# Kernel optimization log

Hardware: AMD Instinct MI355X
Metric: run time of the kernel (lower is better)

The kernel has to match this reference:

```python
import jax, jax.numpy as jnp
import numpy as np

H = 64
N_PERSON = 200000
N_MOVIE = 100000
E_ACTED = 1600000
E_DIRECTED = 200000
E_WWW = 3200000
N_LAYERS = 2


def setup_inputs() -> dict:
    key = jax.random.key(0)
    ks = jax.random.split(key, 24)
    s = 1.0 / np.sqrt(H)
    inp = {
        "x_person": jax.random.normal(ks[0], (N_PERSON, H), jnp.float32),
        "x_movie": jax.random.normal(ks[1], (N_MOVIE, H), jnp.float32),
        "acted_src": jax.random.randint(ks[2], (E_ACTED,), 0, N_PERSON, jnp.int32),
        "acted_dst": jax.random.randint(ks[3], (E_ACTED,), 0, N_MOVIE, jnp.int32),
        "directed_src": jax.random.randint(ks[4], (E_DIRECTED,), 0, N_PERSON, jnp.int32),
        "directed_dst": jax.random.randint(ks[5], (E_DIRECTED,), 0, N_MOVIE, jnp.int32),
        "www_src": jax.random.randint(ks[6], (E_WWW,), 0, N_PERSON, jnp.int32),
        "www_dst": jax.random.randint(ks[7], (E_WWW,), 0, N_PERSON, jnp.int32),
        # per-relation SAGEConv params, stacked over the 2 layers
        "Wl_acted": jax.random.normal(ks[8], (N_LAYERS, H, H), jnp.float32) * s,
        "bl_acted": jnp.zeros((N_LAYERS, H), jnp.float32),
        "Wr_acted": jax.random.normal(ks[9], (N_LAYERS, H, H), jnp.float32) * s,
        "Wl_directed": jax.random.normal(ks[10], (N_LAYERS, H, H), jnp.float32) * s,
        "bl_directed": jnp.zeros((N_LAYERS, H), jnp.float32),
        "Wr_directed": jax.random.normal(ks[11], (N_LAYERS, H, H), jnp.float32) * s,
        "Wl_www": jax.random.normal(ks[12], (N_LAYERS, H, H), jnp.float32) * s,
        "bl_www": jnp.zeros((N_LAYERS, H), jnp.float32),
        "Wr_www": jax.random.normal(ks[13], (N_LAYERS, H, H), jnp.float32) * s,
        "lin_W": jax.random.normal(ks[14], (1, H), jnp.float32) * s,
        "lin_b": jnp.zeros((1,), jnp.float32),
    }
    return inp


def sage_conv(x_src, x_dst, src, dst, Wl, bl, Wr, n_dst):
    # PyG SAGEConv: mean-aggregate source feats at dst, then lin_l(agg) + lin_r(x_dst)
    agg = jax.ops.segment_sum(x_src[src], dst, num_segments=n_dst)  # [n_dst, H_in]
    cnt = jax.ops.segment_sum(jnp.ones((src.shape[0],), x_src.dtype), dst, num_segments=n_dst)
    mean = agg / jnp.maximum(cnt, 1.0)[:, None]
    return mean @ Wl.T + bl + x_dst @ Wr.T


def reference(x_person, x_movie, acted_src, acted_dst, directed_src, directed_dst,
              www_src, www_dst, Wl_acted, bl_acted, Wr_acted,
              Wl_directed, bl_directed, Wr_directed,
              Wl_www, bl_www, Wr_www, lin_W, lin_b):
    x_p, x_m = x_person, x_movie
    for l in range(N_LAYERS):
        # HeteroConv(aggr='sum'): movie receives sum of acted_in and directed convs
        out_m = sage_conv(x_p, x_m, acted_src, acted_dst,
                          Wl_acted[l], bl_acted[l], Wr_acted[l], N_MOVIE)
        out_m = out_m + sage_conv(x_p, x_m, directed_src, directed_dst,
                                  Wl_directed[l], bl_directed[l], Wr_directed[l], N_MOVIE)
        out_p = sage_conv(x_p, x_p, www_src, www_dst,
                          Wl_www[l], bl_www[l], Wr_www[l], N_PERSON)
        x_m = jax.nn.relu(out_m)
        x_p = jax.nn.relu(out_p)
    return (x_m @ lin_W.T + lin_b).squeeze(-1)  # [N_MOVIE]
```

## Files before the change

### kernel.cpp

```cpp
#include <hip/hip_runtime.h>

#define H 64
#define N_PERSON 200000
#define N_MOVIE 100000
#define E_ACTED 1600000
#define E_DIRECTED 200000
#define E_WWW 3200000
#define E_TOTAL (E_ACTED + E_DIRECTED + E_WWW)

#define SH 11
#define NBIN 2048
#define CH 16384

typedef __attribute__((ext_vector_type(8))) short bf16x8;
typedef __attribute__((ext_vector_type(4))) float f32x4;

static __device__ __forceinline__ ushort f2bf(float f) {
  uint u = __float_as_uint(f);
  uint r = (u + 0x7FFFu + ((u >> 16) & 1u)) >> 16;
  return (ushort)r;
}
static __device__ __forceinline__ float bflo(uint u) { return __uint_as_float(u << 16); }
static __device__ __forceinline__ float bfhiq(uint u) { return __uint_as_float(u); }
static __device__ __forceinline__ uint packbf(float lo, float hi) {
  return (uint)f2bf(lo) | ((uint)f2bf(hi) << 16);
}


struct RelP {
  const int* src; const int* dst; int* off;
  int E, N, nblk, nbuk, blkbase, bukbase, cbase, ebase;
};


static __global__ __launch_bounds__(256) void count_cast_k(RelP a, RelP b, RelP c,
                                                           int* __restrict__ counts, int castbase,
                                                           const float* __restrict__ i0,
                                                           ushort* __restrict__ o0, int n0,
                                                           const float* __restrict__ i1,
                                                           ushort* __restrict__ o1, int n1) {
  int blk = blockIdx.x, t = threadIdx.x;
  if (blk >= castbase) {
    int i = (blk - castbase) * 256 + t;
    int stride = 2048 * 256;
    int nt = n0 + n1;
    for (; i < nt; i += stride) {
      const float4* in; ushort4* out; int idx;
      if (i < n0) { in = (const float4*)i0; out = (ushort4*)o0; idx = i; }
      else { in = (const float4*)i1; out = (ushort4*)o1; idx = i - n0; }
      float4 v = in[idx];
      ushort4 o;
      o.x = f2bf(v.x); o.y = f2bf(v.y); o.z = f2bf(v.z); o.w = f2bf(v.w);
      out[idx] = o;
    }
    return;
  }
  __shared__ int hist[128];
  RelP r = (blk >= c.blkbase) ? c : (blk >= b.blkbase) ? b : a;
  int lb = blk - r.blkbase;
  for (int i = t; i < r.nbuk; i += 256) hist[i] = 0;
  __syncthreads();
  int e0 = lb * CH, e1 = min(e0 + CH, r.E);
  for (int e = e0 + t; e < e1; e += 256) atomicAdd(&hist[r.dst[e] >> SH], 1);
  __syncthreads();
  for (int i = t; i < r.nbuk; i += 256) counts[r.cbase + i * r.nblk + lb] = hist[i];
}


static __global__ __launch_bounds__(1024) void scan_one_k(const int* __restrict__ in, int n,
                                                          int* __restrict__ out, int total) {
  __shared__ int wsum[16];
  int t = threadIdx.x;
  int C = (n + 1023) / 1024;
  int i0 = t * C, i1 = min(i0 + C, n);
  int s = 0;
  for (int i = i0; i < i1; ++i) s += in[i];
  int lane = t & 63, w = t >> 6;
  int incl = s;
  for (int d = 1; d < 64; d <<= 1) {
    int v = __shfl_up(incl, d, 64);
    if (lane >= d) incl += v;
  }
  if (lane == 63) wsum[w] = incl;
  __syncthreads();
  if (t == 0) {
    int acc = 0;
    for (int i = 0; i < 16; ++i) { int v = wsum[i]; wsum[i] = acc; acc += v; }
  }
  __syncthreads();
  int run = wsum[w] + (incl - s);
  for (int i = i0; i < i1; ++i) { int v = in[i]; out[i] = run; run += v; }
  if (t == 0) out[n] = total;
}


static __global__ __launch_bounds__(256) void part_scatter_all_k(RelP a, RelP b, RelP c,
                                                                 const int* __restrict__ off_bb,
                                                                 int* __restrict__ pairs) {
  __shared__ int cur[128];
  int blk = blockIdx.x, t = threadIdx.x;
  RelP r = (blk >= c.blkbase) ? c : (blk >= b.blkbase) ? b : a;
  int lb = blk - r.blkbase;
  for (int i = t; i < r.nbuk; i += 256) cur[i] = off_bb[r.cbase + i * r.nblk + lb];
  __syncthreads();
  int e0 = lb * CH, e1 = min(e0 + CH, r.E);
  int e = e0 + t;
  for (; e + 256 < e1; e += 512) {
    int d0 = r.dst[e], s0 = r.src[e];
    int d1 = r.dst[e + 256], s1 = r.src[e + 256];
    int p0 = atomicAdd(&cur[d0 >> SH], 1);
    int p1 = atomicAdd(&cur[d1 >> SH], 1);
    pairs[p0] = ((d0 & (NBIN - 1)) << 18) | s0;
    pairs[p1] = ((d1 & (NBIN - 1)) << 18) | s1;
  }
  if (e < e1) {
    int d0 = r.dst[e], s0 = r.src[e];
    int p0 = atomicAdd(&cur[d0 >> SH], 1);
    pairs[p0] = ((d0 & (NBIN - 1)) << 18) | s0;
  }
}


static __global__ __launch_bounds__(1024) void fine_sort_all_k(RelP a, RelP b, RelP c,
                                                               const int* __restrict__ off_bb,
                                                               const int* __restrict__ pairs,
                                                               int* __restrict__ csr) {
  __shared__ int hist[NBIN];
  __shared__ int wsum[16];
  int bb = blockIdx.x, t = threadIdx.x;
  RelP r = (bb >= c.bukbase) ? c : (bb >= b.bukbase) ? b : a;
  int bkt = bb - r.bukbase;
  int bstart = off_bb[r.cbase + bkt * r.nblk];
  int bend = (bkt + 1 < r.nbuk) ? off_bb[r.cbase + (bkt + 1) * r.nblk] : (r.ebase + r.E);
  int base = bkt << SH;
  int b0 = t * 2, b1 = t * 2 + 1;
  hist[b0] = 0; hist[b1] = 0;
  __syncthreads();
  for (int e = bstart + t; e < bend; e += 1024) atomicAdd(&hist[((uint)pairs[e]) >> 18], 1);
  __syncthreads();
  int h0 = hist[b0], h1 = hist[b1];
  int s = h0 + h1;
  int lane = t & 63, w = t >> 6;
  int incl = s;
  for (int d = 1; d < 64; d <<= 1) {
    int v = __shfl_up(incl, d, 64);
    if (lane >= d) incl += v;
  }
  if (lane == 63) wsum[w] = incl;
  __syncthreads();
  if (t == 0) {
    int acc = 0;
    for (int i = 0; i < 16; ++i) { int v = wsum[i]; wsum[i] = acc; acc += v; }
  }
  __syncthreads();
  int excl = wsum[w] + (incl - s);
  int ex0 = excl, ex1 = excl + h0;
  if (base + b0 < r.N) r.off[base + b0] = bstart + ex0;
  if (base + b1 < r.N) r.off[base + b1] = bstart + ex1;
  if (bkt == r.nbuk - 1 && t == 0) r.off[r.N] = r.ebase + r.E;
  hist[b0] = ex0; hist[b1] = ex1;
  __syncthreads();
  for (int e = bstart + t; e < bend; e += 1024) {
    int p = pairs[e];
    int pos = bstart + atomicAdd(&hist[((uint)p) >> 18], 1);
    csr[pos] = p & 0x3FFFF;
  }
}


struct PullT { const ushort* xsrc; const int* off; ushort* mean; int n; int blkbase; };

#define ACC8(u)                                  \
  do {                                           \
    a0 += bflo((u).x); a1 += bfhiq((u).x);       \
    a2 += bflo((u).y); a3 += bfhiq((u).y);       \
    a4 += bflo((u).z); a5 += bfhiq((u).z);       \
    a6 += bflo((u).w); a7 += bfhiq((u).w);       \
  } while (0)

static __global__ __launch_bounds__(256) void pull_all_k(PullT t0, PullT t1, PullT t2,
                                                         const int* __restrict__ csr) {
  int blk = blockIdx.x;
  PullT tk;
  if (t2.n > 0 && blk >= t2.blkbase) tk = t2;
  else if (blk >= t1.blkbase) tk = t1;
  else tk = t0;
  int lane = threadIdx.x & 63;
  int g = lane >> 3;
  int fo = lane & 7;
  int d = ((blk - tk.blkbase) * 4 + (threadIdx.x >> 6)) * 8 + g;
  bool dok = d < tk.n;
  int dd = dok ? d : (tk.n - 1);
  int e0 = tk.off[dd];
  int e1 = tk.off[dd + 1];
  int cnt = dok ? (e1 - e0) : 0;
  int mx = cnt;
  mx = max(mx, __shfl_xor(mx, 8, 64));
  mx = max(mx, __shfl_xor(mx, 16, 64));
  mx = max(mx, __shfl_xor(mx, 32, 64));

  const ushort* __restrict__ xrow = tk.xsrc + fo * 8;
  float a0 = 0.f, a1 = 0.f, a2 = 0.f, a3 = 0.f, a4 = 0.f, a5 = 0.f, a6 = 0.f, a7 = 0.f;

  int i = 0;
  for (; i + 2 <= mx; i += 2) {
    if (i + 1 < cnt) {
      int s0 = csr[e0 + i];
      int s1 = csr[e0 + i + 1];
      uint4 u0 = *(const uint4*)(xrow + (size_t)s0 * 64);
      uint4 u1 = *(const uint4*)(xrow + (size_t)s1 * 64);
      ACC8(u0); ACC8(u1);
    } else if (i < cnt) {
      int s0 = csr[e0 + i];
      uint4 u0 = *(const uint4*)(xrow + (size_t)s0 * 64);
      ACC8(u0);
    }
  }
  if (i < mx && i < cnt) {
    int s0 = csr[e0 + i];
    uint4 u0 = *(const uint4*)(xrow + (size_t)s0 * 64);
    ACC8(u0);
  }

  if (dok) {
    float inv = 1.0f / fmaxf((float)cnt, 1.0f);
    uint4 o;
    o.x = packbf(a0 * inv, a1 * inv);
    o.y = packbf(a2 * inv, a3 * inv);
    o.z = packbf(a4 * inv, a5 * inv);
    o.w = packbf(a6 * inv, a7 * inv);
    *(uint4*)(tk.mean + (size_t)d * 64 + fo * 8) = o;
  }
}


struct GemmT {
  const ushort *A0, *A1, *A2;
  const float *W0, *W1, *W2, *Wadd, *b0, *b1;
  ushort* outB;
  const float *projW, *projb;
  float* projOut;
  int M, nsrc, blkbase;
};

static __global__ __launch_bounds__(256) void gemm_all_k(GemmT g0, GemmT g1) {
  GemmT g = (g1.M > 0 && (int)blockIdx.x >= g1.blkbase) ? g1 : g0;
  __shared__ ushort Wt[3][64][72];
  const int t = threadIdx.x;
  const int w = t >> 6;
  const int l = t & 63;
  const int lr = l & 15;
  const int lk = l >> 4;
  const int m0 = ((int)blockIdx.x - g.blkbase) * 256;

  auto stageW = [&](const float* W, int s, const float* Wa) {
#pragma unroll
    for (int i = 0; i < 8; ++i) {
      int dp = t + i * 256;
      int j = dp >> 5;
      int kk = (dp & 31) * 2;
      float2 wv = *(const float2*)(W + j * 64 + kk);
      if (Wa) {
        float2 av = *(const float2*)(Wa + j * 64 + kk);
        wv.x += av.x; wv.y += av.y;
      }
      *(uint*)&Wt[s][j][kk] = packbf(wv.x, wv.y);
    }
  };
  stageW(g.W0, 0, nullptr);
  stageW(g.W1, 1, g.nsrc == 2 ? g.Wadd : nullptr);
  if (g.nsrc > 2) stageW(g.W2, 2, g.Wadd);
  __syncthreads();

  f32x4 acc[4][4];
#pragma unroll
  for (int mt = 0; mt < 4; ++mt)
#pragma unroll
    for (int jt = 0; jt < 4; ++jt) acc[mt][jt] = (f32x4){0.f, 0.f, 0.f, 0.f};

  auto doSrc = [&](const ushort* A, int s) {
    bf16x8 aF[4][2];
#pragma unroll
    for (int mt = 0; mt < 4; ++mt) {
      int m = m0 + w * 64 + mt * 16 + lr;
      const ushort* ap = A + (size_t)(m < g.M ? m : 0) * 64 + lk * 8;
      aF[mt][0] = *(const bf16x8*)(ap);
      aF[mt][1] = *(const bf16x8*)(ap + 32);
    }
#pragma unroll
    for (int jt = 0; jt < 4; ++jt) {
#pragma unroll
      for (int k0 = 0; k0 < 2; ++k0) {
        bf16x8 bF = *(const bf16x8*)&Wt[s][jt * 16 + lr][k0 * 32 + lk * 8];
#pragma unroll
        for (int mt = 0; mt < 4; ++mt)
          acc[mt][jt] =
              __builtin_amdgcn_mfma_f32_16x16x32_bf16(bF, aF[mt][k0], acc[mt][jt], 0, 0, 0);
      }
    }
  };
  doSrc(g.A0, 0);
  doSrc(g.A1, 1);
  if (g.nsrc > 2) doSrc(g.A2, 2);

  f32x4 bv[4];
#pragma unroll
  for (int jt = 0; jt < 4; ++jt) {
    f32x4 b = (f32x4){0.f, 0.f, 0.f, 0.f};
    if (g.b0) b += *(const f32x4*)(g.b0 + jt * 16 + lk * 4);
    if (g.b1) b += *(const f32x4*)(g.b1 + jt * 16 + lk * 4);
    bv[jt] = b;
  }

  if (g.projOut) {
    f32x4 pw[4];
#pragma unroll
    for (int jt = 0; jt < 4; ++jt) pw[jt] = *(const f32x4*)(g.projW + jt * 16 + lk * 4);
    float pb = g.projb[0];
#pragma unroll
    for (int mt = 0; mt < 4; ++mt) {
      float p = 0.f;
#pragma unroll
      for (int jt = 0; jt < 4; ++jt) {
        f32x4 o = acc[mt][jt] + bv[jt];
#pragma unroll
        for (int q = 0; q < 4; ++q) p += fmaxf(o[q], 0.f) * pw[jt][q];
      }
      p += __shfl_xor(p, 16, 64);
      p += __shfl_xor(p, 32, 64);
      int m = m0 + w * 64 + mt * 16 + lr;
      if (lk == 0 && m < g.M) g.projOut[m] = p + pb;
    }
  } else {
#pragma unroll
    for (int mt = 0; mt < 4; ++mt) {
      int m = m0 + w * 64 + mt * 16 + lr;
      if (m < g.M) {
        ushort* row = g.outB + (size_t)m * 64 + lk * 4;
#pragma unroll
        for (int jt = 0; jt < 4; ++jt) {
          f32x4 o = acc[mt][jt] + bv[jt];
          uint2 pk;
          pk.x = packbf(fmaxf(o[0], 0.f), fmaxf(o[1], 0.f));
          pk.y = packbf(fmaxf(o[2], 0.f), fmaxf(o[3], 0.f));
          *(uint2*)(row + jt * 16) = pk;
        }
      }
    }
  }
}


extern "C" void kernel_launch(void* const* d_in, const int* in_sizes, int n_in, void* d_out,
                              int out_size, void* d_ws, size_t ws_size, hipStream_t stream) {
  const float* x_person = (const float*)d_in[0];
  const float* x_movie = (const float*)d_in[1];
  const int* acted_src = (const int*)d_in[2];
  const int* acted_dst = (const int*)d_in[3];
  const int* directed_src = (const int*)d_in[4];
  const int* directed_dst = (const int*)d_in[5];
  const int* www_src = (const int*)d_in[6];
  const int* www_dst = (const int*)d_in[7];
  const float* Wl_acted = (const float*)d_in[8];
  const float* bl_acted = (const float*)d_in[9];
  const float* Wr_acted = (const float*)d_in[10];
  const float* Wl_directed = (const float*)d_in[11];
  const float* bl_directed = (const float*)d_in[12];
  const float* Wr_directed = (const float*)d_in[13];
  const float* Wl_www = (const float*)d_in[14];
  const float* bl_www = (const float*)d_in[15];
  const float* Wr_www = (const float*)d_in[16];
  const float* lin_W = (const float*)d_in[17];
  const float* lin_b = (const float*)d_in[18];
  float* out = (float*)d_out;
  (void)in_sizes; (void)n_in; (void)out_size; (void)ws_size;

  char* base = (char*)d_ws;
  size_t pos = 0;
  auto carve = [&](size_t b) -> void* {
    void* r = base + pos;
    pos += (b + 255) & ~(size_t)255;
    return r;
  };
  int* off_a = (int*)carve((N_MOVIE + 1) * sizeof(int));
  int* off_d = (int*)carve((N_MOVIE + 1) * sizeof(int));
  int* off_w = (int*)carve((N_PERSON + 1) * sizeof(int));
  int* csr_all = (int*)carve((size_t)E_TOTAL * sizeof(int));
  int* pairs = (int*)carve((size_t)E_TOTAL * sizeof(int));
  ushort* xpbf = (ushort*)carve((size_t)N_PERSON * H * sizeof(ushort));
  ushort* xmbf = (ushort*)carve((size_t)N_MOVIE * H * sizeof(ushort));
  ushort* xp0bf = (ushort*)carve((size_t)N_PERSON * H * sizeof(ushort));
  ushort* xm0bf = (ushort*)carve((size_t)N_MOVIE * H * sizeof(ushort));
  ushort* meanAbf = (ushort*)carve((size_t)N_MOVIE * H * sizeof(ushort));
  ushort* meanDbf = (ushort*)carve((size_t)N_MOVIE * H * sizeof(ushort));
  ushort* meanWbf = (ushort*)carve((size_t)N_PERSON * H * sizeof(ushort));

  RelP rA, rD, rW;
  rA.src = acted_src;  rA.dst = acted_dst;  rA.off = off_a;
  rA.E = E_ACTED;      rA.N = N_MOVIE;
  rA.nblk = (E_ACTED + CH - 1) / CH;      rA.nbuk = (N_MOVIE + NBIN - 1) >> SH;
  rD.src = directed_src; rD.dst = directed_dst; rD.off = off_d;
  rD.E = E_DIRECTED;     rD.N = N_MOVIE;
  rD.nblk = (E_DIRECTED + CH - 1) / CH;   rD.nbuk = (N_MOVIE + NBIN - 1) >> SH;
  rW.src = www_src;    rW.dst = www_dst;  rW.off = off_w;
  rW.E = E_WWW;        rW.N = N_PERSON;
  rW.nblk = (E_WWW + CH - 1) / CH;        rW.nbuk = (N_PERSON + NBIN - 1) >> SH;
  rA.blkbase = 0;                 rD.blkbase = rA.nblk;           rW.blkbase = rA.nblk + rD.nblk;
  rA.bukbase = 0;                 rD.bukbase = rA.nbuk;           rW.bukbase = rA.nbuk + rD.nbuk;
  rA.cbase = 0;                   rD.cbase = rA.nbuk * rA.nblk;
  rW.cbase = rD.cbase + rD.nbuk * rD.nblk;
  rA.ebase = 0;                   rD.ebase = E_ACTED;             rW.ebase = E_ACTED + E_DIRECTED;
  const int n_total = rW.cbase + rW.nbuk * rW.nblk;
  const int nblk_total = rW.blkbase + rW.nblk;
  const int nbuk_total = rW.bukbase + rW.nbuk;

  int* counts = (int*)carve((size_t)n_total * sizeof(int));
  int* off_bb = (int*)carve((size_t)(n_total + 1) * sizeof(int));

  count_cast_k<<<nblk_total + 2048, 256, 0, stream>>>(rA, rD, rW, counts, nblk_total, x_person,
                                                      xpbf, N_PERSON * H / 4, x_movie, xmbf,
                                                      N_MOVIE * H / 4);
  scan_one_k<<<1, 1024, 0, stream>>>(counts, n_total, off_bb, E_TOTAL);
  part_scatter_all_k<<<nblk_total, 256, 0, stream>>>(rA, rD, rW, off_bb, pairs);
  fine_sort_all_k<<<nbuk_total, 1024, 0, stream>>>(rA, rD, rW, off_bb, pairs, csr_all);

  const int nbA = (N_MOVIE + 31) / 32, nbD = (N_MOVIE + 31) / 32, nbW = (N_PERSON + 31) / 32;
  const int gmM = (N_MOVIE + 255) / 256, gmP = (N_PERSON + 255) / 256;

  {
    PullT pA = {xpbf, off_a, meanAbf, N_MOVIE, 0};
    PullT pD = {xpbf, off_d, meanDbf, N_MOVIE, nbA};
    PullT pW = {xpbf, off_w, meanWbf, N_PERSON, nbA + nbD};
    pull_all_k<<<nbA + nbD + nbW, 256, 0, stream>>>(pA, pD, pW, csr_all);
  }
  {
    GemmT gM = {meanAbf, meanDbf, xmbf,
                Wl_acted, Wl_directed, Wr_acted, Wr_directed, bl_acted, bl_directed,
                xm0bf, nullptr, nullptr, nullptr, N_MOVIE, 3, 0};
    GemmT gP = {meanWbf, xpbf, nullptr,
                Wl_www, Wr_www, nullptr, nullptr, bl_www, nullptr,
                xp0bf, nullptr, nullptr, nullptr, N_PERSON, 2, gmM};
    gemm_all_k<<<gmM + gmP, 256, 0, stream>>>(gM, gP);
  }
  {
    PullT pA = {xp0bf, off_a, meanAbf, N_MOVIE, 0};
    PullT pD = {xp0bf, off_d, meanDbf, N_MOVIE, nbA};
    PullT pZ = {nullptr, nullptr, nullptr, 0, 0};
    pull_all_k<<<nbA + nbD, 256, 0, stream>>>(pA, pD, pZ, csr_all);
  }
  {
    GemmT gM = {meanAbf, meanDbf, xm0bf,
                Wl_acted + 4096, Wl_directed + 4096, Wr_acted + 4096, Wr_directed + 4096,
                bl_acted + 64, bl_directed + 64,
                nullptr, lin_W, lin_b, out, N_MOVIE, 3, 0};
    GemmT gZ = {nullptr, nullptr, nullptr, nullptr, nullptr, nullptr, nullptr, nullptr, nullptr,
                nullptr, nullptr, nullptr, nullptr, 0, 0, 0};
    gemm_all_k<<<gmM, 256, 0, stream>>>(gM, gZ);
  }
}
```

Measured before the change: 352.9 us.

## Fuse neighbor mean aggregation into GEMM kernel via shared-memory staging

```diff
diff --git a/kernel.cpp b/kernel.cpp
--- a/kernel.cpp
+++ b/kernel.cpp
@@ -168,7 +168,16 @@
 }
 
 
-struct PullT { const ushort* xsrc; const int* off; ushort* mean; int n; int blkbase; };
+struct GemmT {
+  const ushort *A0, *A1, *A2;
+  const int *off0, *off1, *off2;
+  const ushort *gx0, *gx1, *gx2;
+  const float *W0, *W1, *W2, *Wadd, *b0, *b1;
+  ushort* outB;
+  const float *projW, *projb;
+  float* projOut;
+  int M, nsrc, blkbase;
+};
 
 #define ACC8(u)                                  \
   do {                                           \
@@ -178,80 +187,31 @@
     a6 += bflo((u).w); a7 += bfhiq((u).w);       \
   } while (0)
 
-static __global__ __launch_bounds__(256) void pull_all_k(PullT t0, PullT t1, PullT t2,
+#define GATHER1(ii)                                        \
+  do {                                                     \
+    int s_ = csr[e0 + (ii)];                               \
+    uint4 u_ = *(const uint4*)(xrow + (size_t)s_ * 64);    \
+    ACC8(u_);                                              \
+  } while (0)
+
+static __global__ __launch_bounds__(256) void gemm_all_k(GemmT g0, GemmT g1,
                                                          const int* __restrict__ csr) {
-  int blk = blockIdx.x;
-  PullT tk;
-  if (t2.n > 0 && blk >= t2.blkbase) tk = t2;
-  else if (blk >= t1.blkbase) tk = t1;
-  else tk = t0;
-  int lane = threadIdx.x & 63;
-  int g = lane >> 3;
-  int fo = lane & 7;
-  int d = ((blk - tk.blkbase) * 4 + (threadIdx.x >> 6)) * 8 + g;
-  bool dok = d < tk.n;
-  int dd = dok ? d : (tk.n - 1);
-  int e0 = tk.off[dd];
-  int e1 = tk.off[dd + 1];
-  int cnt = dok ? (e1 - e0) : 0;
-  int mx = cnt;
-  mx = max(mx, __shfl_xor(mx, 8, 64));
-  mx = max(mx, __shfl_xor(mx, 16, 64));
-  mx = max(mx, __shfl_xor(mx, 32, 64));
-
-  const ushort* __restrict__ xrow = tk.xsrc + fo * 8;
-  float a0 = 0.f, a1 = 0.f, a2 = 0.f, a3 = 0.f, a4 = 0.f, a5 = 0.f, a6 = 0.f, a7 = 0.f;
-
-  int i = 0;
-  for (; i + 2 <= mx; i += 2) {
-    if (i + 1 < cnt) {
-      int s0 = csr[e0 + i];
-      int s1 = csr[e0 + i + 1];
-      uint4 u0 = *(const uint4*)(xrow + (size_t)s0 * 64);
-      uint4 u1 = *(const uint4*)(xrow + (size_t)s1 * 64);
-      ACC8(u0); ACC8(u1);
-    } else if (i < cnt) {
-      int s0 = csr[e0 + i];
-      uint4 u0 = *(const uint4*)(xrow + (size_t)s0 * 64);
-      ACC8(u0);
-    }
-  }
-  if (i < mx && i < cnt) {
-    int s0 = csr[e0 + i];
-    uint4 u0 = *(const uint4*)(xrow + (size_t)s0 * 64);
-    ACC8(u0);
-  }
-
-  if (dok) {
-    float inv = 1.0f / fmaxf((float)cnt, 1.0f);
-    uint4 o;
-    o.x = packbf(a0 * inv, a1 * inv);
-    o.y = packbf(a2 * inv, a3 * inv);
-    o.z = packbf(a4 * inv, a5 * inv);
-    o.w = packbf(a6 * inv, a7 * inv);
-    *(uint4*)(tk.mean + (size_t)d * 64 + fo * 8) = o;
-  }
-}
-
-
-struct GemmT {
-  const ushort *A0, *A1, *A2;
-  const float *W0, *W1, *W2, *Wadd, *b0, *b1;
-  ushort* outB;
-  const float *projW, *projb;
-  float* projOut;
-  int M, nsrc, blkbase;
-};
-
-static __global__ __launch_bounds__(256) void gemm_all_k(GemmT g0, GemmT g1) {
   GemmT g = (g1.M > 0 && (int)blockIdx.x >= g1.blkbase) ? g1 : g0;
   __shared__ ushort Wt[3][64][72];
+  __shared__ ushort Mb[128][72];
   const int t = threadIdx.x;
   const int w = t >> 6;
   const int l = t & 63;
   const int lr = l & 15;
   const int lk = l >> 4;
-  const int m0 = ((int)blockIdx.x - g.blkbase) * 256;
+  const int gg = l >> 3;
+  const int fo = l & 7;
+  const int m0 = ((int)blockIdx.x - g.blkbase) * 128;
+
+  const ushort* As[3] = {g.A0, g.A1, g.A2};
+  const int* offs[3] = {g.off0, g.off1, g.off2};
+  const ushort* gxs[3] = {g.gx0, g.gx1, g.gx2};
+  const float* Ws[3] = {g.W0, g.W1, g.W2};
 
   auto stageW = [&](const float* W, int s, const float* Wa) {
 #pragma unroll
@@ -270,22 +230,75 @@
   stageW(g.W0, 0, nullptr);
   stageW(g.W1, 1, g.nsrc == 2 ? g.Wadd : nullptr);
   if (g.nsrc > 2) stageW(g.W2, 2, g.Wadd);
-  __syncthreads();
-
-  f32x4 acc[4][4];
-#pragma unroll
-  for (int mt = 0; mt < 4; ++mt)
+
+  f32x4 acc[2][4];
+#pragma unroll
+  for (int mt = 0; mt < 2; ++mt)
 #pragma unroll
     for (int jt = 0; jt < 4; ++jt) acc[mt][jt] = (f32x4){0.f, 0.f, 0.f, 0.f};
 
-  auto doSrc = [&](const ushort* A, int s) {
-    bf16x8 aF[4][2];
-#pragma unroll
-    for (int mt = 0; mt < 4; ++mt) {
-      int m = m0 + w * 64 + mt * 16 + lr;
-      const ushort* ap = A + (size_t)(m < g.M ? m : 0) * 64 + lk * 8;
-      aF[mt][0] = *(const bf16x8*)(ap);
-      aF[mt][1] = *(const bf16x8*)(ap + 32);
+  for (int s = 0; s < g.nsrc; ++s) {
+    bf16x8 aF[2][2];
+    if (offs[s]) {
+      __syncthreads();
+      const int* off = offs[s];
+      const ushort* __restrict__ xrow = gxs[s] + fo * 8;
+      for (int rr = 0; rr < 4; ++rr) {
+        int dl = w * 32 + rr * 8 + gg;
+        int d = m0 + dl;
+        bool dok = d < g.M;
+        int dd = dok ? d : (g.M - 1);
+        int e0 = off[dd];
+        int e1 = off[dd + 1];
+        int cnt = dok ? (e1 - e0) : 0;
+        int mx = cnt;
+        mx = max(mx, __shfl_xor(mx, 8, 64));
+        mx = max(mx, __shfl_xor(mx, 16, 64));
+        mx = max(mx, __shfl_xor(mx, 32, 64));
+        float a0 = 0.f, a1 = 0.f, a2 = 0.f, a3 = 0.f, a4 = 0.f, a5 = 0.f, a6 = 0.f, a7 = 0.f;
+        int i = 0;
+        for (; i + 4 <= mx; i += 4) {
+          if (i + 4 <= cnt) {
+            int s0 = csr[e0 + i], s1 = csr[e0 + i + 1];
+            int s2 = csr[e0 + i + 2], s3 = csr[e0 + i + 3];
+            uint4 u0 = *(const uint4*)(xrow + (size_t)s0 * 64);
+            uint4 u1 = *(const uint4*)(xrow + (size_t)s1 * 64);
+            uint4 u2 = *(const uint4*)(xrow + (size_t)s2 * 64);
+            uint4 u3 = *(const uint4*)(xrow + (size_t)s3 * 64);
+            ACC8(u0); ACC8(u1); ACC8(u2); ACC8(u3);
+          } else if (i < cnt) {
+#pragma unroll
+            for (int k = 0; k < 3; ++k)
+              if (i + k < cnt) GATHER1(i + k);
+          }
+        }
+        for (; i < mx; ++i)
+          if (i < cnt) GATHER1(i);
+        float inv = 1.0f / fmaxf((float)cnt, 1.0f);
+        uint4 o;
+        o.x = packbf(a0 * inv, a1 * inv);
+        o.y = packbf(a2 * inv, a3 * inv);
+        o.z = packbf(a4 * inv, a5 * inv);
+        o.w = packbf(a6 * inv, a7 * inv);
+        *(uint4*)&Mb[dl][fo * 8] = o;
+      }
+      __syncthreads();
+#pragma unroll
+      for (int mt = 0; mt < 2; ++mt) {
+        int row = w * 32 + mt * 16 + lr;
+        aF[mt][0] = *(const bf16x8*)&Mb[row][lk * 8];
+        aF[mt][1] = *(const bf16x8*)&Mb[row][32 + lk * 8];
+      }
+    } else {
+      if (s == 0) __syncthreads();
+      const ushort* A = As[s];
+#pragma unroll
+      for (int mt = 0; mt < 2; ++mt) {
+        int m = m0 + w * 32 + mt * 16 + lr;
+        const ushort* ap = A + (size_t)(m < g.M ? m : 0) * 64 + lk * 8;
+        aF[mt][0] = *(const bf16x8*)(ap);
+        aF[mt][1] = *(const bf16x8*)(ap + 32);
+      }
     }
 #pragma unroll
     for (int jt = 0; jt < 4; ++jt) {
@@ -293,15 +306,12 @@
       for (int k0 = 0; k0 < 2; ++k0) {
         bf16x8 bF = *(const bf16x8*)&Wt[s][jt * 16 + lr][k0 * 32 + lk * 8];
 #pragma unroll
-        for (int mt = 0; mt < 4; ++mt)
+        for (int mt = 0; mt < 2; ++mt)
           acc[mt][jt] =
               __builtin_amdgcn_mfma_f32_16x16x32_bf16(bF, aF[mt][k0], acc[mt][jt], 0, 0, 0);
       }
     }
-  };
-  doSrc(g.A0, 0);
-  doSrc(g.A1, 1);
-  if (g.nsrc > 2) doSrc(g.A2, 2);
+  }
 
   f32x4 bv[4];
 #pragma unroll
@@ -318,7 +328,7 @@
     for (int jt = 0; jt < 4; ++jt) pw[jt] = *(const f32x4*)(g.projW + jt * 16 + lk * 4);
     float pb = g.projb[0];
 #pragma unroll
-    for (int mt = 0; mt < 4; ++mt) {
+    for (int mt = 0; mt < 2; ++mt) {
       float p = 0.f;
 #pragma unroll
       for (int jt = 0; jt < 4; ++jt) {
@@ -328,13 +338,13 @@
       }
       p += __shfl_xor(p, 16, 64);
       p += __shfl_xor(p, 32, 64);
-      int m = m0 + w * 64 + mt * 16 + lr;
+      int m = m0 + w * 32 + mt * 16 + lr;
       if (lk == 0 && m < g.M) g.projOut[m] = p + pb;
     }
   } else {
 #pragma unroll
-    for (int mt = 0; mt < 4; ++mt) {
-      int m = m0 + w * 64 + mt * 16 + lr;
+    for (int mt = 0; mt < 2; ++mt) {
+      int m = m0 + w * 32 + mt * 16 + lr;
       if (m < g.M) {
         ushort* row = g.outB + (size_t)m * 64 + lk * 4;
 #pragma unroll
@@ -391,9 +401,6 @@
   ushort* xmbf = (ushort*)carve((size_t)N_MOVIE * H * sizeof(ushort));
   ushort* xp0bf = (ushort*)carve((size_t)N_PERSON * H * sizeof(ushort));
   ushort* xm0bf = (ushort*)carve((size_t)N_MOVIE * H * sizeof(ushort));
-  ushort* meanAbf = (ushort*)carve((size_t)N_MOVIE * H * sizeof(ushort));
-  ushort* meanDbf = (ushort*)carve((size_t)N_MOVIE * H * sizeof(ushort));
-  ushort* meanWbf = (ushort*)carve((size_t)N_PERSON * H * sizeof(ushort));
 
   RelP rA, rD, rW;
   rA.src = acted_src;  rA.dst = acted_dst;  rA.off = off_a;
@@ -424,37 +431,37 @@
   part_scatter_all_k<<<nblk_total, 256, 0, stream>>>(rA, rD, rW, off_bb, pairs);
   fine_sort_all_k<<<nbuk_total, 1024, 0, stream>>>(rA, rD, rW, off_bb, pairs, csr_all);
 
-  const int nbA = (N_MOVIE + 31) / 32, nbD = (N_MOVIE + 31) / 32, nbW = (N_PERSON + 31) / 32;
-  const int gmM = (N_MOVIE + 255) / 256, gmP = (N_PERSON + 255) / 256;
+  const int gmM = (N_MOVIE + 127) / 128, gmP = (N_PERSON + 127) / 128;
 
   {
-    PullT pA = {xpbf, off_a, meanAbf, N_MOVIE, 0};
-    PullT pD = {xpbf, off_d, meanDbf, N_MOVIE, nbA};
-    PullT pW = {xpbf, off_w, meanWbf, N_PERSON, nbA + nbD};
-    pull_all_k<<<nbA + nbD + nbW, 256, 0, stream>>>(pA, pD, pW, csr_all);
+    GemmT gM{};
+    gM.A2 = xmbf;
+    gM.off0 = off_a; gM.gx0 = xpbf;
+    gM.off1 = off_d; gM.gx1 = xpbf;
+    gM.W0 = Wl_acted; gM.W1 = Wl_directed; gM.W2 = Wr_acted; gM.Wadd = Wr_directed;
+    gM.b0 = bl_acted; gM.b1 = bl_directed;
+    gM.outB = xm0bf;
+    gM.M = N_MOVIE; gM.nsrc = 3; gM.blkbase = 0;
+    GemmT gP{};
+    gP.A1 = xpbf;
+    gP.off0 = off_w; gP.gx0 = xpbf;
+    gP.W0 = Wl_www; gP.W1 = Wr_www;
+    gP.b0 = bl_www;
+    gP.outB = xp0bf;
+    gP.M = N_PERSON; gP.nsrc = 2; gP.blkbase = gmM;
+    gemm_all_k<<<gmM + gmP, 256, 0, stream>>>(gM, gP, csr_all);
   }
   {
-    GemmT gM = {meanAbf, meanDbf, xmbf,
-                Wl_acted, Wl_directed, Wr_acted, Wr_directed, bl_acted, bl_directed,
-                xm0bf, nullptr, nullptr, nullptr, N_MOVIE, 3, 0};
-    GemmT gP = {meanWbf, xpbf, nullptr,
-                Wl_www, Wr_www, nullptr, nullptr, bl_www, nullptr,
-                xp0bf, nullptr, nullptr, nullptr, N_PERSON, 2, gmM};
-    gemm_all_k<<<gmM + gmP, 256, 0, stream>>>(gM, gP);
-  }
-  {
-    PullT pA = {xp0bf, off_a, meanAbf, N_MOVIE, 0};
-    PullT pD = {xp0bf, off_d, meanDbf, N_MOVIE, nbA};
-    PullT pZ = {nullptr, nullptr, nullptr, 0, 0};
-    pull_all_k<<<nbA + nbD, 256, 0, stream>>>(pA, pD, pZ, csr_all);
-  }
-  {
-    GemmT gM = {meanAbf, meanDbf, xm0bf,
-                Wl_acted + 4096, Wl_directed + 4096, Wr_acted + 4096, Wr_directed + 4096,
-                bl_acted + 64, bl_directed + 64,
-                nullptr, lin_W, lin_b, out, N_MOVIE, 3, 0};
-    GemmT gZ = {nullptr, nullptr, nullptr, nullptr, nullptr, nullptr, nullptr, nullptr, nullptr,
-                nullptr, nullptr, nullptr, nullptr, 0, 0, 0};
-    gemm_all_k<<<gmM, 256, 0, stream>>>(gM, gZ);
-  }
-}
+    GemmT gM{};
+    gM.A2 = xm0bf;
+    gM.off0 = off_a; gM.gx0 = xp0bf;
+    gM.off1 = off_d; gM.gx1 = xp0bf;
+    gM.W0 = Wl_acted + 4096; gM.W1 = Wl_directed + 4096;
+    gM.W2 = Wr_acted + 4096; gM.Wadd = Wr_directed + 4096;
+    gM.b0 = bl_acted + 64; gM.b1 = bl_directed + 64;
+    gM.projW = lin_W; gM.projb = lin_b; gM.projOut = out;
+    gM.M = N_MOVIE; gM.nsrc = 3; gM.blkbase = 0;
+    GemmT gZ{};
+    gemm_all_k<<<gmM, 256, 0, stream>>>(gM, gZ, csr_all);
+  }
+}
```

Result: slower. 460.1 us (+30.4%).
